# Performance work log

Hardware: AMD Instinct MI355X
Metric: run time of the kernel (lower is better)

## Reference

```python
import jax, jax.numpy as jnp
import numpy as np

DIM = 768
HEADS = 12
HEAD_DIM = DIM // HEADS


def setup_inputs() -> dict:
    key = jax.random.key(0)
    ks = jax.random.split(key, 6)
    B, Nq, Nkv = 2, 2048, 2048
    s = 0.02
    return {
        "query_source": jax.random.normal(ks[0], (B, Nq, DIM), jnp.float32),
        "kv_source": jax.random.normal(ks[1], (B, Nkv, DIM), jnp.float32),
        "Wq": jax.random.normal(ks[2], (DIM, DIM), jnp.float32) * s,
        "Wkv": jax.random.normal(ks[3], (DIM, 2 * DIM), jnp.float32) * s,
        "Wproj": jax.random.normal(ks[4], (DIM, DIM), jnp.float32) * s,
        "bproj": jax.random.normal(ks[5], (DIM,), jnp.float32) * s,
    }


def reference(query_source, kv_source, Wq, Wkv, Wproj, bproj):
    B, Nq, D = query_source.shape
    Nkv = kv_source.shape[1]
    scale = HEAD_DIM ** -0.5
    # projections (qkv_bias=False)
    q = (query_source @ Wq).reshape(B, Nq, HEADS, HEAD_DIM)
    kv = (kv_source @ Wkv).reshape(B, Nkv, 2, HEADS, HEAD_DIM)
    k, v = kv[:, :, 0], kv[:, :, 1]  # (B, Nkv, H, Dh)
    # scores: (B, H, Nq, Nkv)
    attn = jnp.einsum("bqhd,bkhd->bhqk", q, k) * scale
    attn = jax.nn.softmax(attn, axis=-1)
    # attn_drop = 0 (eval)
    x = jnp.einsum("bhqk,bkhd->bqhd", attn, v).reshape(B, Nq, D)
    return x @ Wproj + bproj
```

## Files before the change

kernel.cpp:

```cpp
#include <hip/hip_runtime.h>
#include <math.h>
#include <stdint.h>

typedef __bf16 bf16_t;
typedef __attribute__((ext_vector_type(8))) __bf16 bf16x8;
typedef __attribute__((ext_vector_type(4))) __bf16 bf16x4;
typedef __attribute__((ext_vector_type(4))) float f32x4;

#define DIM   768
#define HEADS 12
#define HD    64
#define NB    2
#define NQ    2048
#define NKV   2048
#define MROWS 4096
#define NQKV  2304

__device__ __forceinline__ float fast_exp2(float x)
{
#if __has_builtin(__builtin_amdgcn_exp2f)
    return __builtin_amdgcn_exp2f(x);
#else
    return exp2f(x);
#endif
}

__device__ __forceinline__ uint32_t pack_bf16x2(float a, float b)
{
    const uint32_t lo = __builtin_bit_cast(uint32_t, a) + 0x8000u;
    const uint32_t hi = __builtin_bit_cast(uint32_t, b) + 0x8000u;
#if __has_builtin(__builtin_amdgcn_perm)
    return __builtin_amdgcn_perm(hi, lo, 0x07060302u);
#else
    return (lo >> 16) | (hi & 0xffff0000u);
#endif
}

__device__ __forceinline__ void async_copy16(const bf16_t* g, bf16_t* l)
{
    typedef const __attribute__((address_space(1))) uint32_t* gp_t;
    typedef __attribute__((address_space(3))) uint32_t* lp_t;
    __builtin_amdgcn_global_load_lds((gp_t)(const void*)g, (lp_t)(void*)l, 16, 0, 0);
}

__global__ void prep_kernel(const float* __restrict__ qs, bf16_t* __restrict__ qs_bf,
                            const float* __restrict__ kvs, bf16_t* __restrict__ kvs_bf,
                            const float* __restrict__ Wq, const float* __restrict__ Wkv,
                            const float* __restrict__ Wproj, bf16_t* __restrict__ Wt,
                            float escale)
{
    __shared__ float tile[32][33];
    const int z = blockIdx.z;
    if (z < 2) {
        const float* in  = z ? kvs : qs;
        bf16_t*      out = z ? kvs_bf : qs_bf;
        const int i = (blockIdx.x * 256 + threadIdx.x) * 8;
        bf16x8 v;
#pragma unroll
        for (int j = 0; j < 8; j++) v[j] = (bf16_t)in[i + j];
        *(bf16x8*)(out + i) = v;
        return;
    }
    const int N   = (z == 3) ? 2 * DIM : DIM;
    const int nb  = N / 32;
    const int idx = blockIdx.x;
    if (idx >= nb * (DIM / 32)) return;
    const float* W = (z == 2) ? Wq : (z == 3) ? Wkv : Wproj;
    bf16_t* T = Wt + ((z == 2) ? (size_t)0 : (z == 3) ? (size_t)DIM * DIM
                                                      : (size_t)NQKV * DIM);
    const float scl = (z == 2) ? escale : 1.0f;
    const int n0 = (idx % nb) * 32, k0 = (idx / nb) * 32;
    const int tx = threadIdx.x & 31, ty = threadIdx.x >> 5;
#pragma unroll
    for (int i = 0; i < 4; i++)
        tile[ty + i * 8][tx] = W[(size_t)(k0 + ty + i * 8) * N + n0 + tx];
    __syncthreads();
#pragma unroll
    for (int i = 0; i < 4; i++)
        T[(size_t)(n0 + ty + i * 8) * DIM + k0 + tx] = (bf16_t)(tile[tx][ty + i * 8] * scl);
}

template<int MODE, int TN>
__global__ __launch_bounds__(256)
void gemm_bk64(const bf16_t* __restrict__ Aq, const bf16_t* __restrict__ Akv,
               const bf16_t* __restrict__ Bt,
               bf16_t* __restrict__ Qb, bf16_t* __restrict__ Kb, bf16_t* __restrict__ Vtb,
               float* __restrict__ ofp, const float* __restrict__ bias)
{
    constexpr int K  = DIM;
    constexpr int NT = TN / 32;
    constexpr int ABLK = 128 * 64;
    constexpr int BBLK = TN * 64;
    constexpr int SELEMS = (MODE == 0) ? (128 * 136) : (ABLK + BBLK);
    __shared__ __align__(16) bf16_t smem[SELEMS];
    bf16_t* As = smem;
    bf16_t* Bs = smem + ABLK;

    const int tid  = threadIdx.x;
    const int wave = tid >> 6, lane = tid & 63;
    const int quad = lane >> 4, l16 = lane & 15, l7 = l16 & 7;
    const int bm = blockIdx.x * 128, bn = blockIdx.y * TN;
    const int wm = (wave >> 1) * 64, wn = (wave & 1) * (TN / 2);

    const bf16_t* A = (MODE == 0) ? (bn < DIM ? Aq : Akv) : Aq;

    const int srow = tid >> 3;
    const int scol = ((tid & 7) ^ (srow & 7)) * 8;
    const bf16_t* Ag[4];
    const bf16_t* Bg[NT];
#pragma unroll
    for (int i = 0; i < 4; i++)
        Ag[i] = A + (size_t)(bm + i * 32 + srow) * K + scol;
#pragma unroll
    for (int i = 0; i < NT; i++)
        Bg[i] = Bt + (size_t)(bn + i * 32 + srow) * K + scol;
    bf16_t* AsL = As + tid * 8;
    bf16_t* BsL = Bs + tid * 8;

    f32x4 acc[4][NT] = {};

    for (int k0 = 0; k0 < K; k0 += 64) {
#pragma unroll
        for (int i = 0; i < 4; i++) async_copy16(Ag[i] + k0, AsL + i * 2048);
#pragma unroll
        for (int i = 0; i < NT; i++) async_copy16(Bg[i] + k0, BsL + i * 2048);
        __syncthreads();
#pragma unroll
        for (int ks = 0; ks < 2; ks++) {
            const int pc = ((ks * 4 + quad) ^ l7) * 8;
            bf16x8 af[4], bfr[NT];
#pragma unroll
            for (int mt = 0; mt < 4; mt++)
                af[mt] = *(const bf16x8*)(&As[(wm + mt * 16 + l16) * 64 + pc]);
#pragma unroll
            for (int nt = 0; nt < NT; nt++)
                bfr[nt] = *(const bf16x8*)(&Bs[(wn + nt * 16 + l16) * 64 + pc]);
#pragma unroll
            for (int mt = 0; mt < 4; mt++)
#pragma unroll
                for (int nt = 0; nt < NT; nt++)
                    acc[mt][nt] = __builtin_amdgcn_mfma_f32_16x16x32_bf16(
                        af[mt], bfr[nt], acc[mt][nt], 0, 0, 0);
        }
        __syncthreads();
    }

    if (MODE == 1) {
#pragma unroll
        for (int mt = 0; mt < 4; mt++)
#pragma unroll
            for (int nt = 0; nt < NT; nt++)
#pragma unroll
                for (int r = 0; r < 4; r++) {
                    const int gm = bm + wm + mt * 16 + quad * 4 + r;
                    const int gn = bn + wn + nt * 16 + l16;
                    ofp[(size_t)gm * DIM + gn] = acc[mt][nt][r] + bias[gn];
                }
    } else if (bn < DIM) {
#pragma unroll
        for (int mt = 0; mt < 4; mt++)
#pragma unroll
            for (int nt = 0; nt < NT; nt++)
#pragma unroll
                for (int r = 0; r < 4; r++) {
                    const int gm = bm + wm + mt * 16 + quad * 4 + r;
                    const int gn = bn + wn + nt * 16 + l16;
                    Qb[(size_t)gm * DIM + gn] = (bf16_t)acc[mt][nt][r];
                }
    } else if (bn < 2 * DIM) {
#pragma unroll
        for (int mt = 0; mt < 4; mt++)
#pragma unroll
            for (int nt = 0; nt < NT; nt++)
#pragma unroll
                for (int r = 0; r < 4; r++) {
                    const int gm = bm + wm + mt * 16 + quad * 4 + r;
                    const int gn = bn + wn + nt * 16 + l16 - DIM;
                    Kb[(size_t)gm * DIM + gn] = (bf16_t)acc[mt][nt][r];
                }
    } else {
        bf16_t* tr = smem;
#pragma unroll
        for (int mt = 0; mt < 4; mt++)
#pragma unroll
            for (int nt = 0; nt < NT; nt++) {
                bf16x4 tv;
#pragma unroll
                for (int r = 0; r < 4; r++) tv[r] = (bf16_t)acc[mt][nt][r];
                *(bf16x4*)(&tr[(wn + nt * 16 + l16) * 136 + wm + mt * 16 + quad * 4]) = tv;
            }
        __syncthreads();
        const int b = bm >> 11, kv0 = bm & 2047;
        const int n2base = bn - 2 * DIM;
        const int cg = tid & 15, cc = cg >> 2, cq = cg & 3;
#pragma unroll
        for (int i = 0; i < TN / 16; i++) {
            const int row = i * 16 + (tid >> 4);
            const int n2 = n2base + row, h = n2 >> 6, d = n2 & 63;
            const bf16x4 lo4 = *(const bf16x4*)(&tr[row * 136 + cc * 32 + cq * 4]);
            const bf16x4 hi4 = *(const bf16x4*)(&tr[row * 136 + cc * 32 + 16 + cq * 4]);
            bf16x8 vv;
#pragma unroll
            for (int j = 0; j < 4; j++) { vv[j] = lo4[j]; vv[4 + j] = hi4[j]; }
            *(bf16x8*)(Vtb + ((size_t)(b * HEADS + h) * HD + d) * NKV + kv0 + cg * 8) = vv;
        }
    }
}

__global__ __launch_bounds__(256, 4)
void attn_kernel(const bf16_t* __restrict__ Qb, const bf16_t* __restrict__ Kb,
                 const bf16_t* __restrict__ Vt, bf16_t* __restrict__ Xb)
{
    __shared__ __align__(16) bf16_t kvbuf[16384];
    __shared__ float libuf[4][2][16];

    const int tid  = threadIdx.x;
    const int wave = tid >> 6, lane = tid & 63;
    const int quad = lane >> 4, l16 = lane & 15;
    const int l7   = l16 & 7;
    const int qh = wave & 1, kvh = wave >> 1;
    const int bh = blockIdx.x;
    const int b = bh / HEADS, h = bh % HEADS;
    const int q0 = blockIdx.y * 64;

    const bf16_t* Qp = Qb + (size_t)b * NQ * DIM + h * HD;
    const bf16_t* Kp = Kb + (size_t)b * NKV * DIM + h * HD;
    const bf16_t* Vp = Vt + (size_t)(b * HEADS + h) * HD * NKV;

    bf16x8 qf[2][2];
#pragma unroll
    for (int qt = 0; qt < 2; qt++)
#pragma unroll
        for (int ks = 0; ks < 2; ks++)
            qf[qt][ks] = *(const bf16x8*)(Qp + (size_t)(q0 + qh * 32 + qt * 16 + l16) * DIM
                                          + ks * 32 + quad * 8);

    const int kl8 = lane >> 3;
    const bf16_t* Kg0 = Kp + (size_t)(wave * 32 + kl8) * DIM + (((lane & 7) ^ kl8) * 8);
    const int vl4 = lane >> 4, vp = lane & 15;
    const bf16_t* Vg0[4];
#pragma unroll
    for (int i = 0; i < 4; i++) {
        const int d = wave * 16 + i * 4 + vl4;
        const int c = (vp & 8) | ((vp & 7) ^ (d & 7));
        Vg0[i] = Vp + (size_t)d * NKV + c * 8;
    }
    bf16_t* KgL = kvbuf + wave * 2048 + lane * 8;
    bf16_t* VgL = kvbuf + 8192 + wave * 2048 + lane * 8;

    f32x4 o[4][2] = {};
    float li[2] = {0.0f, 0.0f};

    for (int t = 0; t < NKV / 128; t++) {
        const int kv0 = t * 128;
#pragma unroll
        for (int i = 0; i < 4; i++)
            async_copy16(Kg0 + (size_t)(kv0 + i * 8) * DIM, KgL + i * 512);
#pragma unroll
        for (int i = 0; i < 4; i++)
            async_copy16(Vg0[i] + kv0, VgL + i * 512);
        __syncthreads();

        f32x4 s[4][2] = {};
#pragma unroll
        for (int kt = 0; kt < 4; kt++)
#pragma unroll
            for (int ks = 0; ks < 2; ks++) {
                const bf16x8 kf = *(const bf16x8*)(&kvbuf[
                    (kvh * 64 + kt * 16 + l16) * 64 + ((((ks << 2) | quad) ^ l7) * 8)]);
#pragma unroll
                for (int qt = 0; qt < 2; qt++)
                    s[kt][qt] = __builtin_amdgcn_mfma_f32_16x16x32_bf16(
                        kf, qf[qt][ks], s[kt][qt], 0, 0, 0);
            }

        bf16x8 pb[2][2];
#pragma unroll
        for (int qt = 0; qt < 2; qt++) {
            float p[16];
#pragma unroll
            for (int kt = 0; kt < 4; kt++)
#pragma unroll
                for (int r = 0; r < 4; r++) p[kt * 4 + r] = fast_exp2(s[kt][qt][r]);
            float rs = 0.0f;
#pragma unroll
            for (int j = 0; j < 16; j++) rs += p[j];
            li[qt] += rs;
#pragma unroll
            for (int kc = 0; kc < 2; kc++) {
                union { uint32_t u[4]; bf16x8 v; } pu;
#pragma unroll
                for (int i = 0; i < 4; i++)
                    pu.u[i] = pack_bf16x2(p[kc * 8 + 2 * i], p[kc * 8 + 2 * i + 1]);
                pb[qt][kc] = pu.v;
            }
        }

#pragma unroll
        for (int dt = 0; dt < 4; dt++) {
            const int droff = 8192 + (dt * 16 + l16) * 128;
#pragma unroll
            for (int kc = 0; kc < 2; kc++) {
                const bf16x8 vf = *(const bf16x8*)(&kvbuf[
                    droff + (kvh * 8 + ((kc * 4 + quad) ^ l7)) * 8]);
#pragma unroll
                for (int qt = 0; qt < 2; qt++)
                    o[dt][qt] = __builtin_amdgcn_mfma_f32_16x16x32_bf16(
                        vf, pb[qt][kc], o[dt][qt], 0, 0, 0);
            }
        }
        __syncthreads();
    }

#pragma unroll
    for (int qt = 0; qt < 2; qt++) {
        li[qt] += __shfl_xor(li[qt], 16);
        li[qt] += __shfl_xor(li[qt], 32);
    }
    if (quad == 0) { libuf[wave][0][l16] = li[0]; libuf[wave][1][l16] = li[1]; }

    float* ob = (float*)(kvbuf + qh * 8192);
    if (kvh == 1) {
#pragma unroll
        for (int dt = 0; dt < 4; dt++)
#pragma unroll
            for (int qt = 0; qt < 2; qt++)
#pragma unroll
                for (int r = 0; r < 4; r++)
                    ob[(dt * 16 + quad * 4 + r) * 33 + qt * 16 + l16] = o[dt][qt][r];
    }
    __syncthreads();
    if (kvh == 0) {
        const float inv0 = 1.0f / (li[0] + libuf[2 + qh][0][l16]);
        const float inv1 = 1.0f / (li[1] + libuf[2 + qh][1][l16]);
#pragma unroll
        for (int dt = 0; dt < 4; dt++)
#pragma unroll
            for (int qt = 0; qt < 2; qt++)
#pragma unroll
                for (int r = 0; r < 4; r++)
                    o[dt][qt][r] = (o[dt][qt][r]
                                    + ob[(dt * 16 + quad * 4 + r) * 33 + qt * 16 + l16])
                                   * (qt ? inv1 : inv0);
    }
    __syncthreads();
    bf16_t* Ob16 = kvbuf;
    if (kvh == 0) {
#pragma unroll
        for (int dt = 0; dt < 4; dt++)
#pragma unroll
            for (int qt = 0; qt < 2; qt++) {
                bf16x4 ov;
#pragma unroll
                for (int r = 0; r < 4; r++) ov[r] = (bf16_t)o[dt][qt][r];
                *(bf16x4*)(&Ob16[(qh * 32 + qt * 16 + l16) * 72 + dt * 16 + quad * 4]) = ov;
            }
    }
    __syncthreads();
    {
        const int row = tid >> 2, ch = (tid & 3) * 16;
        bf16_t* dst = Xb + (size_t)(b * NQ + q0 + row) * DIM + h * HD + ch;
        *(bf16x8*)(dst)     = *(const bf16x8*)(&Ob16[row * 72 + ch]);
        *(bf16x8*)(dst + 8) = *(const bf16x8*)(&Ob16[row * 72 + ch + 8]);
    }
}

extern "C" void kernel_launch(void* const* d_in, const int* in_sizes, int n_in,
                              void* d_out, int out_size, void* d_ws, size_t ws_size,
                              hipStream_t stream)
{
    const float* qs    = (const float*)d_in[0];
    const float* kvs   = (const float*)d_in[1];
    const float* Wq    = (const float*)d_in[2];
    const float* Wkv   = (const float*)d_in[3];
    const float* Wproj = (const float*)d_in[4];
    const float* bproj = (const float*)d_in[5];
    float* out = (float*)d_out;

    bf16_t* w = (bf16_t*)d_ws;
    bf16_t* qs_bf  = w;  w += (size_t)MROWS * DIM;
    bf16_t* kvs_bf = w;  w += (size_t)MROWS * DIM;
    bf16_t* Wt     = w;  w += (size_t)NQKV * DIM;
    bf16_t* Wprojt = w;  w += (size_t)DIM * DIM;
    bf16_t* Qb     = w;  w += (size_t)MROWS * DIM;
    bf16_t* Kb     = w;  w += (size_t)MROWS * DIM;
    bf16_t* Vtb    = w;  w += (size_t)MROWS * DIM;
    bf16_t* Xb     = qs_bf;

    const float escale = 0.125f * 1.44269504088896341f;
    prep_kernel<<<dim3(MROWS * DIM / 2048, 1, 5), 256, 0, stream>>>(
        qs, qs_bf, kvs, kvs_bf, Wq, Wkv, Wproj, Wt, escale);

    gemm_bk64<0, 96><<<dim3(MROWS / 128, NQKV / 96), 256, 0, stream>>>(
        qs_bf, kvs_bf, Wt, Qb, Kb, Vtb, nullptr, nullptr);
    attn_kernel<<<dim3(NB * HEADS, NQ / 64), 256, 0, stream>>>(Qb, Kb, Vtb, Xb);
    gemm_bk64<1, 32><<<dim3(MROWS / 128, DIM / 32), 256, 0, stream>>>(
        Xb, nullptr, Wprojt, nullptr, nullptr, nullptr, out, bproj);
}
```

Before: 155.9 us.

## Double-buffer K/V tiles in attention kernel and raise MFMA wave priority

The attention kernel now keeps two LDS buffers for K/V tiles. It loads the first tile before the loop and, on each iteration, issues the async copy for the next tile before computing on the current one, so global loads overlap the MFMA and softmax work. It also wraps the MFMA sections in s_setprio calls to favour waves issuing matrix ops. This doubles the LDS footprint, and the launch bound drops from 4 to 2 blocks per CU, which lowers occupancy and may leave the grid's blocks scheduled in more rounds.

```diff
diff --git a/kernel.cpp b/kernel.cpp
--- a/kernel.cpp
+++ b/kernel.cpp
@@ -207,12 +207,13 @@
     }
 }
 
-__global__ __launch_bounds__(256, 4)
+__global__ __launch_bounds__(256, 2)
 void attn_kernel(const bf16_t* __restrict__ Qb, const bf16_t* __restrict__ Kb,
                  const bf16_t* __restrict__ Vt, bf16_t* __restrict__ Xb)
 {
-    __shared__ __align__(16) bf16_t kvbuf[16384];
+    __shared__ __align__(16) bf16_t kvbuf[2][16384];
     __shared__ float libuf[4][2][16];
+    bf16_t* kvflat = &kvbuf[0][0];
 
     const int tid  = threadIdx.x;
     const int wave = tid >> 6, lane = tid & 63;
@@ -227,14 +228,6 @@
     const bf16_t* Kp = Kb + (size_t)b * NKV * DIM + h * HD;
     const bf16_t* Vp = Vt + (size_t)(b * HEADS + h) * HD * NKV;
 
-    bf16x8 qf[2][2];
-#pragma unroll
-    for (int qt = 0; qt < 2; qt++)
-#pragma unroll
-        for (int ks = 0; ks < 2; ks++)
-            qf[qt][ks] = *(const bf16x8*)(Qp + (size_t)(q0 + qh * 32 + qt * 16 + l16) * DIM
-                                          + ks * 32 + quad * 8);
-
     const int kl8 = lane >> 3;
     const bf16_t* Kg0 = Kp + (size_t)(wave * 32 + kl8) * DIM + (((lane & 7) ^ kl8) * 8);
     const int vl4 = lane >> 4, vp = lane & 15;
@@ -245,34 +238,59 @@
         const int c = (vp & 8) | ((vp & 7) ^ (d & 7));
         Vg0[i] = Vp + (size_t)d * NKV + c * 8;
     }
-    bf16_t* KgL = kvbuf + wave * 2048 + lane * 8;
-    bf16_t* VgL = kvbuf + 8192 + wave * 2048 + lane * 8;
+    const int loff = wave * 2048 + lane * 8;
+
+    {
+        bf16_t* kb = kvbuf[0] + loff;
+        bf16_t* vb = kvbuf[0] + 8192 + loff;
+#pragma unroll
+        for (int i = 0; i < 4; i++) async_copy16(Kg0 + (size_t)(i * 8) * DIM, kb + i * 512);
+#pragma unroll
+        for (int i = 0; i < 4; i++) async_copy16(Vg0[i], vb + i * 512);
+    }
+
+    bf16x8 qf[2][2];
+#pragma unroll
+    for (int qt = 0; qt < 2; qt++)
+#pragma unroll
+        for (int ks = 0; ks < 2; ks++)
+            qf[qt][ks] = *(const bf16x8*)(Qp + (size_t)(q0 + qh * 32 + qt * 16 + l16) * DIM
+                                          + ks * 32 + quad * 8);
 
     f32x4 o[4][2] = {};
     float li[2] = {0.0f, 0.0f};
 
+    __syncthreads();
+
     for (int t = 0; t < NKV / 128; t++) {
-        const int kv0 = t * 128;
-#pragma unroll
-        for (int i = 0; i < 4; i++)
-            async_copy16(Kg0 + (size_t)(kv0 + i * 8) * DIM, KgL + i * 512);
-#pragma unroll
-        for (int i = 0; i < 4; i++)
-            async_copy16(Vg0[i] + kv0, VgL + i * 512);
-        __syncthreads();
+        const bf16_t* kv = kvbuf[t & 1];
+
+        if (t + 1 < NKV / 128) {
+            bf16_t* kb = kvbuf[(t & 1) ^ 1] + loff;
+            bf16_t* vb = kvbuf[(t & 1) ^ 1] + 8192 + loff;
+            const int kv1 = (t + 1) * 128;
+#pragma unroll
+            for (int i = 0; i < 4; i++)
+                async_copy16(Kg0 + (size_t)(kv1 + i * 8) * DIM, kb + i * 512);
+#pragma unroll
+            for (int i = 0; i < 4; i++)
+                async_copy16(Vg0[i] + kv1, vb + i * 512);
+        }
 
         f32x4 s[4][2] = {};
+        __builtin_amdgcn_s_setprio(1);
 #pragma unroll
         for (int kt = 0; kt < 4; kt++)
 #pragma unroll
             for (int ks = 0; ks < 2; ks++) {
-                const bf16x8 kf = *(const bf16x8*)(&kvbuf[
+                const bf16x8 kf = *(const bf16x8*)(&kv[
                     (kvh * 64 + kt * 16 + l16) * 64 + ((((ks << 2) | quad) ^ l7) * 8)]);
 #pragma unroll
                 for (int qt = 0; qt < 2; qt++)
                     s[kt][qt] = __builtin_amdgcn_mfma_f32_16x16x32_bf16(
                         kf, qf[qt][ks], s[kt][qt], 0, 0, 0);
             }
+        __builtin_amdgcn_s_setprio(0);
 
         bf16x8 pb[2][2];
 #pragma unroll
@@ -296,12 +314,13 @@
             }
         }
 
+        __builtin_amdgcn_s_setprio(1);
 #pragma unroll
         for (int dt = 0; dt < 4; dt++) {
             const int droff = 8192 + (dt * 16 + l16) * 128;
 #pragma unroll
             for (int kc = 0; kc < 2; kc++) {
-                const bf16x8 vf = *(const bf16x8*)(&kvbuf[
+                const bf16x8 vf = *(const bf16x8*)(&kv[
                     droff + (kvh * 8 + ((kc * 4 + quad) ^ l7)) * 8]);
 #pragma unroll
                 for (int qt = 0; qt < 2; qt++)
@@ -309,6 +328,8 @@
                         vf, pb[qt][kc], o[dt][qt], 0, 0, 0);
             }
         }
+        __builtin_amdgcn_s_setprio(0);
+
         __syncthreads();
     }
 
@@ -319,7 +340,7 @@
     }
     if (quad == 0) { libuf[wave][0][l16] = li[0]; libuf[wave][1][l16] = li[1]; }
 
-    float* ob = (float*)(kvbuf + qh * 8192);
+    float* ob = (float*)(kvflat + qh * 8192);
     if (kvh == 1) {
 #pragma unroll
         for (int dt = 0; dt < 4; dt++)
@@ -344,7 +365,7 @@
                                    * (qt ? inv1 : inv0);
     }
     __syncthreads();
-    bf16_t* Ob16 = kvbuf;
+    bf16_t* Ob16 = kvflat;
     if (kvh == 0) {
 #pragma unroll
         for (int dt = 0; dt < 4; dt++)
```

After: 171.7 us. 1.1x slower.
